# Performance work log

Measured on AMD Instinct MI355X. Metric: run time of the kernel, lower is better.

Reference implementation:

```python
import jax, jax.numpy as jnp
import numpy as np

EPS = 1e-8

@jax.custom_vjp
def spike(x):
    # Heaviside forward, SuperSpike surrogate gradient in backward
    return (x > 0.0).astype(x.dtype)

def _spike_fwd(x):
    return spike(x), x

def _spike_bwd(x, g):
    return (g / (1.0 + 10.0 * jnp.abs(x)) ** 2,)

spike.defvjp(_spike_fwd, _spike_bwd)


def setup_inputs() -> dict:
    key = jax.random.key(0)
    k1, k2, k3, k4 = jax.random.split(key, 4)
    B, T, I, O = 128, 128, 1024, 1024
    x = jax.random.normal(k1, (B, T, I), dtype=jnp.float32)
    # w ~ N(0, 1/sqrt(I)) per reset_parameters
    w = jax.random.normal(k2, (I, O), dtype=jnp.float32) * np.float32(1.0 / np.sqrt(I))
    # beta ~ N(0.7, 0.01), clamped to [0,1]
    beta = jnp.clip(0.7 + 0.01 * jax.random.normal(k3, (1,), dtype=jnp.float32), 0.0, 1.0)
    # b ~ N(1.0, 0.01), clamped to >= 0
    b = jnp.clip(1.0 + 0.01 * jax.random.normal(k4, (1024,), dtype=jnp.float32), 0.0, None)
    return {"x": x, "w": w, "beta": beta, "b": b}


def reference(x, w, beta, b):
    # x: [B, T, I]; w: [I, O]; beta: [1]; b: [O]
    h = jnp.einsum('btc,cd->btd', x, w)                 # [B, T, O]
    d = jnp.einsum('ab,ac->bc', w, w)                    # lateral reset matrix [O, O]
    norm = (w ** 2).sum(0)                               # [O]
    inv_norm = 1.0 / (norm + EPS)
    B, O = x.shape[0], w.shape[1]

    def step(carry, h_t):
        mem, spk = carry
        rst = spk @ d                                    # [B, O]
        mem = (mem - rst) * beta + h_t * (1.0 - beta)
        mthr = mem * inv_norm - b
        spk = spike(mthr)
        return (mem, spk), spk

    init = (jnp.zeros((B, O), x.dtype), jnp.zeros((B, O), x.dtype))
    _, spk_rec = jax.lax.scan(step, init, jnp.swapaxes(h, 0, 1))  # [T, B, O]
    spk_rec = jnp.swapaxes(spk_rec, 0, 1)                # [B, T, O]
    loss = 0.5 * (spk_rec ** 2).mean()
    return spk_rec, loss
```

## Files before the change

kernel.cpp:

```cpp
#include <hip/hip_runtime.h>
#include <hip/hip_fp16.h>

#define B_ 128
#define T_ 128
#define I_ 1024
#define O_ 1024
#define M_ (B_*T_)
#define NOUT (M_*O_)

typedef __attribute__((ext_vector_type(8))) _Float16 half8;
typedef __attribute__((ext_vector_type(4))) float floatx4;

__device__ __forceinline__ void gld_lds16(const void* g, void* l) {
    __builtin_amdgcn_global_load_lds((const __attribute__((address_space(1))) void*)g,
                                     (__attribute__((address_space(3))) void*)l,
                                     16, 0, 0);
}

__device__ __forceinline__ void barrier_lds_only() {
    asm volatile("" ::: "memory");
    __builtin_amdgcn_s_waitcnt(0xC07F);
    __builtin_amdgcn_s_barrier();
    asm volatile("" ::: "memory");
}

__device__ __forceinline__ void split3h(float x, unsigned short& h,
                                        unsigned short& m, unsigned short& l) {
    __half f0 = __float2half(x);
    float r1 = x - __half2float(f0);
    __half f1 = __float2half(r1);
    float r2 = r1 - __half2float(f1);
    __half f2 = __float2half(r2);
    h = __half_as_ushort(f0);
    m = __half_as_ushort(f1);
    l = __half_as_ushort(f2);
}

__global__ __launch_bounds__(256) void split_x(const float* __restrict__ X,
                                               unsigned short* __restrict__ Xh,
                                               unsigned short* __restrict__ Xm,
                                               unsigned short* __restrict__ Xl) {
    size_t base = ((size_t)blockIdx.x * 256 + threadIdx.x) * 4;
    float4 v = *(const float4*)(X + base);
    ushort4 hh, mm, ll;
    split3h(v.x, hh.x, mm.x, ll.x);
    split3h(v.y, hh.y, mm.y, ll.y);
    split3h(v.z, hh.z, mm.z, ll.z);
    split3h(v.w, hh.w, mm.w, ll.w);
    *(ushort4*)(Xh + base) = hh;
    *(ushort4*)(Xm + base) = mm;
    *(ushort4*)(Xl + base) = ll;
}

__global__ __launch_bounds__(256) void split_wt(const float* __restrict__ W,
                                                unsigned short* __restrict__ WTh,
                                                unsigned short* __restrict__ WTm,
                                                unsigned short* __restrict__ WTl) {
    __shared__ float t[64][65];
    const int tid = threadIdx.x;
    const int tx = tid & 63, ty4 = tid >> 6;
    const int r0 = blockIdx.x * 64, c0 = blockIdx.y * 64;
#pragma unroll
    for (int j = 0; j < 16; ++j) {
        int row = j * 4 + ty4;
        t[row][tx] = W[(size_t)(r0 + row) * O_ + c0 + tx];
    }
    __syncthreads();
#pragma unroll
    for (int j = 0; j < 16; ++j) {
        int i = j * 4 + ty4;
        float v = t[tx][i];
        unsigned short h, m, l;
        split3h(v, h, m, l);
        size_t off = (size_t)(c0 + i) * I_ + r0 + tx;
        WTh[off] = h; WTm[off] = m; WTl[off] = l;
    }
}

__global__ __launch_bounds__(512, 2) void gemm_h_mfma(
        const unsigned short* __restrict__ Xh, const unsigned short* __restrict__ Xm,
        const unsigned short* __restrict__ Xl, const unsigned short* __restrict__ WTh,
        const unsigned short* __restrict__ WTm, const unsigned short* __restrict__ WTl,
        float* __restrict__ H) {
    const int K = I_, N = O_;
    __shared__ unsigned short P[2][36864];

    const int tid = threadIdx.x;
    const int lane = tid & 63;
    const int wid = tid >> 6;
    const int wrow = wid >> 2;
    const int wcol = wid & 3;
    const int l15 = lane & 15, quad = lane >> 4;
    const int bm = blockIdx.x * 128, bn = blockIdx.y * 256;

    const int srow = tid >> 2, sch = tid & 3;
    const int schg = sch ^ ((srow >> 1) & 3);
    const unsigned short* gsrcA[3];
    const unsigned short* gsrcB[3];
    gsrcA[0] = Xh  + (size_t)(bm + srow) * K + schg * 8;
    gsrcA[1] = Xm  + (size_t)(bm + srow) * K + schg * 8;
    gsrcA[2] = Xl  + (size_t)(bm + srow) * K + schg * 8;
    gsrcB[0] = WTh + (size_t)(bn + srow) * K + schg * 8;
    gsrcB[1] = WTm + (size_t)(bn + srow) * K + schg * 8;
    gsrcB[2] = WTl + (size_t)(bn + srow) * K + schg * 8;

    auto stage = [&](int kt) {
        unsigned short* wb = &P[0][0] + (size_t)(kt & 1) * 36864;
        const size_t k0 = (size_t)kt * 32;
#pragma unroll
        for (int p = 0; p < 3; ++p)
            gld_lds16(gsrcA[p] + k0, wb + p * 4096 + tid * 8);
#pragma unroll
        for (int p = 0; p < 3; ++p) {
            unsigned short* bb = wb + 12288 + p * 8192 + tid * 8;
            gld_lds16(gsrcB[p] + k0, bb);
            gld_lds16(gsrcB[p] + (size_t)128 * K + k0, bb + 4096);
        }
    };

    floatx4 acc[4][4];
#pragma unroll
    for (int mt = 0; mt < 4; ++mt)
#pragma unroll
        for (int nt = 0; nt < 4; ++nt) acc[mt][nt] = (floatx4)(0.f);

    stage(0);

    for (int kt = 0; kt < 32; ++kt) {
        const unsigned short* rb = &P[0][0] + (size_t)(kt & 1) * 36864;

        asm volatile("" ::: "memory");
        __builtin_amdgcn_s_waitcnt(0x1F70);
        __builtin_amdgcn_s_barrier();
        asm volatile("" ::: "memory");

        half8 Af[3][4];
#pragma unroll
        for (int pa = 0; pa < 3; ++pa)
#pragma unroll
            for (int mt = 0; mt < 4; ++mt) {
                const int row = wrow * 64 + mt * 16 + l15;
                const int chk = quad ^ ((row >> 1) & 3);
                Af[pa][mt] = *(const half8*)(rb + pa * 4096 + row * 32 + chk * 8);
            }

        if (kt < 31) stage(kt + 1);

#pragma unroll
        for (int pb = 0; pb < 3; ++pb) {
            half8 Bf[4];
#pragma unroll
            for (int nt = 0; nt < 4; ++nt) {
                const int col = wcol * 64 + nt * 16 + l15;
                const int chk = quad ^ ((col >> 1) & 3);
                Bf[nt] = *(const half8*)(rb + 12288 + pb * 8192 + col * 32 + chk * 8);
            }
#pragma unroll
            for (int nt = 0; nt < 4; ++nt)
#pragma unroll
                for (int mt = 0; mt < 4; ++mt) {
                    acc[mt][nt] = __builtin_amdgcn_mfma_f32_16x16x32_f16(Af[0][mt], Bf[nt], acc[mt][nt], 0, 0, 0);
                    if (pb < 2)
                        acc[mt][nt] = __builtin_amdgcn_mfma_f32_16x16x32_f16(Af[1][mt], Bf[nt], acc[mt][nt], 0, 0, 0);
                    if (pb == 0)
                        acc[mt][nt] = __builtin_amdgcn_mfma_f32_16x16x32_f16(Af[2][mt], Bf[nt], acc[mt][nt], 0, 0, 0);
                }
        }
    }

#pragma unroll
    for (int mt = 0; mt < 4; ++mt)
#pragma unroll
        for (int nt = 0; nt < 4; ++nt) {
            int grow = bm + wrow * 64 + mt * 16 + quad * 4;
            int gcol = bn + wcol * 64 + nt * 16 + l15;
            float* hp = H + (size_t)grow * N + gcol;
#pragma unroll
            for (int r = 0; r < 4; ++r) hp[(size_t)r * N] = acc[mt][nt][r];
        }
}

__global__ __launch_bounds__(256) void gemm_wtw(const float* __restrict__ W,
                                                float* __restrict__ D) {
    const int K = I_, N = O_;
    __shared__ float As[32][68];
    __shared__ float Bs[32][68];
    const int tid = threadIdx.x;
    const int tx = tid & 15, ty = tid >> 4;
    const int bj = blockIdx.x * 64, bo = blockIdx.y * 64;
    const int lr = tid >> 4;
    const int lc = (tid & 15) << 2;

    float acc[4][4];
#pragma unroll
    for (int m = 0; m < 4; m++)
#pragma unroll
        for (int n = 0; n < 4; n++) acc[m][n] = 0.f;

    for (int k0 = 0; k0 < K; k0 += 32) {
        float4 a0 = *(const float4*)(W + (size_t)(k0 + lr) * N + bj + lc);
        float4 a1 = *(const float4*)(W + (size_t)(k0 + lr + 16) * N + bj + lc);
        float4 b0 = *(const float4*)(W + (size_t)(k0 + lr) * N + bo + lc);
        float4 b1 = *(const float4*)(W + (size_t)(k0 + lr + 16) * N + bo + lc);
        __syncthreads();
        *(float4*)&As[lr][lc] = a0; *(float4*)&As[lr + 16][lc] = a1;
        *(float4*)&Bs[lr][lc] = b0; *(float4*)&Bs[lr + 16][lc] = b1;
        __syncthreads();
#pragma unroll
        for (int k = 0; k < 32; ++k) {
            float4 av = *(const float4*)&As[k][ty * 4];
            float4 bv = *(const float4*)&Bs[k][tx * 4];
            float am[4] = {av.x, av.y, av.z, av.w};
            float bb[4] = {bv.x, bv.y, bv.z, bv.w};
#pragma unroll
            for (int m = 0; m < 4; m++)
#pragma unroll
                for (int n = 0; n < 4; n++) acc[m][n] += am[m] * bb[n];
        }
    }
#pragma unroll
    for (int m = 0; m < 4; m++) {
        float4 v = make_float4(acc[m][0], acc[m][1], acc[m][2], acc[m][3]);
        *(float4*)(D + (size_t)(bj + ty * 4 + m) * N + bo + tx * 4) = v;
    }
}

__global__ void colnorm_diag(const float* __restrict__ D, float* __restrict__ invn,
                             unsigned int* __restrict__ counter,
                             float* __restrict__ zrow) {
    int o = blockIdx.x * 256 + threadIdx.x;
    if (o == 0) *counter = 0u;
    invn[o] = 1.0f / (D[(size_t)o * O_ + o] + 1e-8f);
    zrow[o] = 0.0f;
}

__global__ __launch_bounds__(512) void scan_kernel(const float* __restrict__ h,
                                                   const float* __restrict__ d,
                                                   const float* __restrict__ invn,
                                                   const float* __restrict__ bias,
                                                   const float* __restrict__ beta,
                                                   const float* __restrict__ zrow,
                                                   float* __restrict__ out,
                                                   unsigned int* __restrict__ spike_count) {
    __shared__ int lst[2][O_];
    __shared__ int cnt[T_ + 1];
    __shared__ unsigned int red[512];

    const int tid = threadIdx.x;
    const int lane = tid & 63;
    const int b = blockIdx.x;
    const int o2 = tid * 2;
    const float betav = beta[0];
    const float omb = 1.0f - betav;

    const float2 invn2 = *(const float2*)(invn + o2);
    const float2 b2 = *(const float2*)(bias + o2);
    float2 mem2 = make_float2(0.f, 0.f);

    for (int i = tid; i <= T_; i += 512) cnt[i] = 0;
    unsigned int local_count = 0;
    const float* hb = h + (size_t)b * T_ * O_;
    float* ob = out + (size_t)b * T_ * O_;
    const float* zp = zrow + o2;
    const unsigned long long below = (lane == 63) ? 0xFFFFFFFFFFFFFFFFull >> 1
                                                  : ((1ull << lane) - 1ull);

    float2 hcur = *(const float2*)(hb + o2);
    __syncthreads();

    for (int t = 0; t < T_; ++t) {
        const int p = t & 1, q = p ^ 1;
        const int n = cnt[t];

        float2 hnext = make_float2(0.f, 0.f);
        if (t + 1 < T_) hnext = *(const float2*)(hb + (size_t)(t + 1) * O_ + o2);

        float2 rst = make_float2(0.f, 0.f);
        for (int i = 0; i < n; i += 8) {
            float2 v[8];
#pragma unroll
            for (int u = 0; u < 8; ++u) {
                const int idx = i + u;
                const int j = lst[p][idx & (O_ - 1)];
                const float* src = (idx < n) ? (d + (size_t)j * O_ + o2) : zp;
                v[u] = *(const float2*)src;
            }
#pragma unroll
            for (int u = 0; u < 8; ++u) { rst.x += v[u].x; rst.y += v[u].y; }
        }

        mem2.x = (mem2.x - rst.x) * betav + hcur.x * omb;
        mem2.y = (mem2.y - rst.y) * betav + hcur.y * omb;

        const int s0 = (mem2.x * invn2.x - b2.x) > 0.0f;
        const int s1 = (mem2.y * invn2.y - b2.y) > 0.0f;

        float2 sv = make_float2(s0 ? 1.f : 0.f, s1 ? 1.f : 0.f);
        *(float2*)(ob + (size_t)t * O_ + o2) = sv;
        local_count += (unsigned)(s0 + s1);

        unsigned long long mk0 = __ballot(s0);
        unsigned long long mk1 = __ballot(s1);
        const int c0 = __popcll(mk0);
        const int tot = c0 + __popcll(mk1);
        int base = 0;
        if (lane == 0 && tot) base = atomicAdd(&cnt[t + 1], tot);
        base = __shfl(base, 0, 64);
        if (s0) lst[q][base + __popcll(mk0 & below)] = o2 + 0;
        base += c0;
        if (s1) lst[q][base + __popcll(mk1 & below)] = o2 + 1;

        barrier_lds_only();
        hcur = hnext;
    }

    red[tid] = local_count;
    __syncthreads();
    for (int st = 256; st > 0; st >>= 1) {
        if (tid < st) red[tid] += red[tid + st];
        __syncthreads();
    }
    if (tid == 0) atomicAdd(spike_count, red[0]);
}

__global__ void finalize_loss(const unsigned int* __restrict__ spike_count,
                              float* __restrict__ loss_out) {
    *loss_out = 0.5f * ((float)(*spike_count) / 16777216.0f);
}

extern "C" void kernel_launch(void* const* d_in, const int* in_sizes, int n_in,
                              void* d_out, int out_size, void* d_ws, size_t ws_size,
                              hipStream_t stream) {
    const float* x    = (const float*)d_in[0];
    const float* w    = (const float*)d_in[1];
    const float* beta = (const float*)d_in[2];
    const float* bias = (const float*)d_in[3];
    float* out = (float*)d_out;

    char* ws = (char*)d_ws;
    float* h    = (float*)ws;
    float* dmat = (float*)(ws + (size_t)67108864);
    float* invn = (float*)(ws + (size_t)71303168);
    unsigned int* cntp = (unsigned int*)(ws + (size_t)71307264);
    unsigned short* wt_h = (unsigned short*)(ws + (size_t)71311360);
    unsigned short* wt_m = (unsigned short*)(ws + (size_t)73408512);
    unsigned short* wt_l = (unsigned short*)(ws + (size_t)75505664);
    unsigned short* x_h  = (unsigned short*)(ws + (size_t)77602816);
    unsigned short* x_m  = (unsigned short*)(ws + (size_t)111157248);
    unsigned short* x_l  = (unsigned short*)(ws + (size_t)144711680);
    float* zrow = (float*)x_h;

    split_x<<<M_ * I_ / 1024, 256, 0, stream>>>(x, x_h, x_m, x_l);
    split_wt<<<dim3(I_ / 64, O_ / 64), 256, 0, stream>>>(w, wt_h, wt_m, wt_l);
    gemm_h_mfma<<<dim3(M_ / 128, O_ / 256), 512, 0, stream>>>(x_h, x_m, x_l,
                                                              wt_h, wt_m, wt_l, h);
    gemm_wtw<<<dim3(O_ / 64, O_ / 64), 256, 0, stream>>>(w, dmat);
    colnorm_diag<<<O_ / 256, 256, 0, stream>>>(dmat, invn, cntp, zrow);
    scan_kernel<<<B_, 512, 0, stream>>>(h, dmat, invn, bias, beta, zrow, out, cntp);
    finalize_loss<<<1, 1, 0, stream>>>(cntp, out + (size_t)NOUT);
}
```

Measured before the change: 465.6 us.

## Run scan with one wavefront per batch row using ballot-based spike lists

The scan kernel shrinks from 512 threads per batch row to a single 64-lane wavefront that owns all 1024 outputs (16 per lane). Spike indices are no longer written to an LDS list with atomics and block barriers. Each lane keeps a 16-bit spike mask, and the wave walks the spikes through ballot and readlane. This removes per-timestep block barriers and LDS traffic, but each block now issues far fewer concurrent loads. Only 128 wavefronts cover the whole GPU, so hiding latency on the gathered rows of d gets harder.

```diff
diff --git a/kernel.cpp b/kernel.cpp
--- a/kernel.cpp
+++ b/kernel.cpp
@@ -15,13 +15,6 @@
     __builtin_amdgcn_global_load_lds((const __attribute__((address_space(1))) void*)g,
                                      (__attribute__((address_space(3))) void*)l,
                                      16, 0, 0);
-}
-
-__device__ __forceinline__ void barrier_lds_only() {
-    asm volatile("" ::: "memory");
-    __builtin_amdgcn_s_waitcnt(0xC07F);
-    __builtin_amdgcn_s_barrier();
-    asm volatile("" ::: "memory");
 }
 
 __device__ __forceinline__ void split3h(float x, unsigned short& h,
@@ -234,93 +227,112 @@
     zrow[o] = 0.0f;
 }
 
-__global__ __launch_bounds__(512) void scan_kernel(const float* __restrict__ h,
-                                                   const float* __restrict__ d,
-                                                   const float* __restrict__ invn,
-                                                   const float* __restrict__ bias,
-                                                   const float* __restrict__ beta,
-                                                   const float* __restrict__ zrow,
-                                                   float* __restrict__ out,
-                                                   unsigned int* __restrict__ spike_count) {
-    __shared__ int lst[2][O_];
-    __shared__ int cnt[T_ + 1];
-    __shared__ unsigned int red[512];
-
-    const int tid = threadIdx.x;
-    const int lane = tid & 63;
+__global__ __launch_bounds__(64) void scan_kernel(const float* __restrict__ h,
+                                                  const float* __restrict__ d,
+                                                  const float* __restrict__ invn,
+                                                  const float* __restrict__ bias,
+                                                  const float* __restrict__ beta,
+                                                  const float* __restrict__ zrow,
+                                                  float* __restrict__ out,
+                                                  unsigned int* __restrict__ spike_count) {
+    const int lane = threadIdx.x;
     const int b = blockIdx.x;
-    const int o2 = tid * 2;
     const float betav = beta[0];
     const float omb = 1.0f - betav;
-
-    const float2 invn2 = *(const float2*)(invn + o2);
-    const float2 b2 = *(const float2*)(bias + o2);
-    float2 mem2 = make_float2(0.f, 0.f);
-
-    for (int i = tid; i <= T_; i += 512) cnt[i] = 0;
-    unsigned int local_count = 0;
+    const int base0 = lane * 4;
+
+    float4 mem[4], invn4[4], b4[4], hcur[4], hnext[4];
+#pragma unroll
+    for (int g = 0; g < 4; ++g) {
+        mem[g] = make_float4(0.f, 0.f, 0.f, 0.f);
+        invn4[g] = *(const float4*)(invn + base0 + g * 256);
+        b4[g]   = *(const float4*)(bias + base0 + g * 256);
+    }
     const float* hb = h + (size_t)b * T_ * O_;
     float* ob = out + (size_t)b * T_ * O_;
-    const float* zp = zrow + o2;
-    const unsigned long long below = (lane == 63) ? 0xFFFFFFFFFFFFFFFFull >> 1
-                                                  : ((1ull << lane) - 1ull);
-
-    float2 hcur = *(const float2*)(hb + o2);
-    __syncthreads();
+#pragma unroll
+    for (int g = 0; g < 4; ++g) hcur[g] = *(const float4*)(hb + base0 + g * 256);
+
+    unsigned int lm = 0u;
+    unsigned int local_count = 0u;
 
     for (int t = 0; t < T_; ++t) {
-        const int p = t & 1, q = p ^ 1;
-        const int n = cnt[t];
-
-        float2 hnext = make_float2(0.f, 0.f);
-        if (t + 1 < T_) hnext = *(const float2*)(hb + (size_t)(t + 1) * O_ + o2);
-
-        float2 rst = make_float2(0.f, 0.f);
-        for (int i = 0; i < n; i += 8) {
-            float2 v[8];
-#pragma unroll
-            for (int u = 0; u < 8; ++u) {
-                const int idx = i + u;
-                const int j = lst[p][idx & (O_ - 1)];
-                const float* src = (idx < n) ? (d + (size_t)j * O_ + o2) : zp;
-                v[u] = *(const float2*)src;
+        if (t + 1 < T_) {
+#pragma unroll
+            for (int g = 0; g < 4; ++g)
+                hnext[g] = *(const float4*)(hb + (size_t)(t + 1) * O_ + base0 + g * 256);
+        } else {
+#pragma unroll
+            for (int g = 0; g < 4; ++g) hnext[g] = make_float4(0.f, 0.f, 0.f, 0.f);
+        }
+
+        float4 rst[4];
+#pragma unroll
+        for (int g = 0; g < 4; ++g) rst[g] = make_float4(0.f, 0.f, 0.f, 0.f);
+
+        unsigned long long am = __ballot(lm != 0u);
+        unsigned int cl = 0u;
+        unsigned int clm = 0u;
+        while (am != 0ull || clm != 0u) {
+            const float* srcb[8];
+#pragma unroll
+            for (int k = 0; k < 8; ++k) {
+                while (clm == 0u && am != 0ull) {
+                    cl = (unsigned)__builtin_ctzll(am);
+                    am &= am - 1ull;
+                    clm = (unsigned)__builtin_amdgcn_readlane((int)lm, (int)cl) & 0xFFFFu;
+                }
+                if (clm != 0u) {
+                    const int bbit = __builtin_ctz(clm);
+                    clm &= clm - 1u;
+                    const int j = ((bbit >> 2) << 8) + ((int)cl << 2) + (bbit & 3);
+                    srcb[k] = d + (size_t)j * O_;
+                } else {
+                    srcb[k] = zrow;
+                }
             }
-#pragma unroll
-            for (int u = 0; u < 8; ++u) { rst.x += v[u].x; rst.y += v[u].y; }
-        }
-
-        mem2.x = (mem2.x - rst.x) * betav + hcur.x * omb;
-        mem2.y = (mem2.y - rst.y) * betav + hcur.y * omb;
-
-        const int s0 = (mem2.x * invn2.x - b2.x) > 0.0f;
-        const int s1 = (mem2.y * invn2.y - b2.y) > 0.0f;
-
-        float2 sv = make_float2(s0 ? 1.f : 0.f, s1 ? 1.f : 0.f);
-        *(float2*)(ob + (size_t)t * O_ + o2) = sv;
-        local_count += (unsigned)(s0 + s1);
-
-        unsigned long long mk0 = __ballot(s0);
-        unsigned long long mk1 = __ballot(s1);
-        const int c0 = __popcll(mk0);
-        const int tot = c0 + __popcll(mk1);
-        int base = 0;
-        if (lane == 0 && tot) base = atomicAdd(&cnt[t + 1], tot);
-        base = __shfl(base, 0, 64);
-        if (s0) lst[q][base + __popcll(mk0 & below)] = o2 + 0;
-        base += c0;
-        if (s1) lst[q][base + __popcll(mk1 & below)] = o2 + 1;
-
-        barrier_lds_only();
-        hcur = hnext;
-    }
-
-    red[tid] = local_count;
-    __syncthreads();
-    for (int st = 256; st > 0; st >>= 1) {
-        if (tid < st) red[tid] += red[tid + st];
-        __syncthreads();
-    }
-    if (tid == 0) atomicAdd(spike_count, red[0]);
+            float4 vv[8][4];
+#pragma unroll
+            for (int k = 0; k < 8; ++k)
+#pragma unroll
+                for (int g = 0; g < 4; ++g)
+                    vv[k][g] = *(const float4*)(srcb[k] + base0 + g * 256);
+#pragma unroll
+            for (int k = 0; k < 8; ++k)
+#pragma unroll
+                for (int g = 0; g < 4; ++g) {
+                    rst[g].x += vv[k][g].x; rst[g].y += vv[k][g].y;
+                    rst[g].z += vv[k][g].z; rst[g].w += vv[k][g].w;
+                }
+        }
+
+        unsigned int nlm = 0u;
+#pragma unroll
+        for (int g = 0; g < 4; ++g) {
+            mem[g].x = (mem[g].x - rst[g].x) * betav + hcur[g].x * omb;
+            mem[g].y = (mem[g].y - rst[g].y) * betav + hcur[g].y * omb;
+            mem[g].z = (mem[g].z - rst[g].z) * betav + hcur[g].z * omb;
+            mem[g].w = (mem[g].w - rst[g].w) * betav + hcur[g].w * omb;
+            const int s0 = (mem[g].x * invn4[g].x - b4[g].x) > 0.0f;
+            const int s1 = (mem[g].y * invn4[g].y - b4[g].y) > 0.0f;
+            const int s2 = (mem[g].z * invn4[g].z - b4[g].z) > 0.0f;
+            const int s3 = (mem[g].w * invn4[g].w - b4[g].w) > 0.0f;
+            nlm |= ((unsigned)s0 << (g * 4 + 0)) | ((unsigned)s1 << (g * 4 + 1)) |
+                   ((unsigned)s2 << (g * 4 + 2)) | ((unsigned)s3 << (g * 4 + 3));
+            float4 sv = make_float4(s0 ? 1.f : 0.f, s1 ? 1.f : 0.f,
+                                    s2 ? 1.f : 0.f, s3 ? 1.f : 0.f);
+            *(float4*)(ob + (size_t)t * O_ + base0 + g * 256) = sv;
+            local_count += (unsigned)(s0 + s1 + s2 + s3);
+        }
+        lm = nlm;
+#pragma unroll
+        for (int g = 0; g < 4; ++g) hcur[g] = hnext[g];
+    }
+
+#pragma unroll
+    for (int off = 32; off > 0; off >>= 1)
+        local_count += (unsigned)__shfl_down((int)local_count, off, 64);
+    if (lane == 0) atomicAdd(spike_count, local_count);
 }
 
 __global__ void finalize_loss(const unsigned int* __restrict__ spike_count,
@@ -356,6 +368,6 @@
                                                               wt_h, wt_m, wt_l, h);
     gemm_wtw<<<dim3(O_ / 64, O_ / 64), 256, 0, stream>>>(w, dmat);
     colnorm_diag<<<O_ / 256, 256, 0, stream>>>(dmat, invn, cntp, zrow);
-    scan_kernel<<<B_, 512, 0, stream>>>(h, dmat, invn, bias, beta, zrow, out, cntp);
+    scan_kernel<<<B_, 64, 0, stream>>>(h, dmat, invn, bias, beta, zrow, out, cntp);
     finalize_loss<<<1, 1, 0, stream>>>(cntp, out + (size_t)NOUT);
 }
```

After: 645.7 us. +38.7%, slower.

## Process two batch rows per scan block to share barriers and interleave loads

Applied to the files above, without the earlier changes.

The scan kernel now handles two independent batch rows (b and b+64) in each 512-thread block, launching half as many blocks. The two recurrences are interleaved so the gathered reset-matrix row loads for both can be in flight together, and one barrier per timestep serves both rows. The aim is more memory-level parallelism and fewer barriers across the latency-bound serial scan. The costs are fewer blocks (64 on a many-CU GPU), more registers and LDS per block, and a reset loop whose trip count is the larger of the two spike counts.

```diff
diff --git a/kernel.cpp b/kernel.cpp
--- a/kernel.cpp
+++ b/kernel.cpp
@@ -242,76 +242,109 @@
                                                    const float* __restrict__ zrow,
                                                    float* __restrict__ out,
                                                    unsigned int* __restrict__ spike_count) {
-    __shared__ int lst[2][O_];
-    __shared__ int cnt[T_ + 1];
+    __shared__ int lstA[2][O_], lstB[2][O_];
+    __shared__ int cntA[T_ + 1], cntB[T_ + 1];
     __shared__ unsigned int red[512];
 
     const int tid = threadIdx.x;
     const int lane = tid & 63;
-    const int b = blockIdx.x;
+    const int bA = blockIdx.x;
+    const int bB = blockIdx.x + 64;
     const int o2 = tid * 2;
     const float betav = beta[0];
     const float omb = 1.0f - betav;
 
     const float2 invn2 = *(const float2*)(invn + o2);
     const float2 b2 = *(const float2*)(bias + o2);
-    float2 mem2 = make_float2(0.f, 0.f);
-
-    for (int i = tid; i <= T_; i += 512) cnt[i] = 0;
+    float2 memA = make_float2(0.f, 0.f), memB = make_float2(0.f, 0.f);
+
+    for (int i = tid; i <= T_; i += 512) { cntA[i] = 0; cntB[i] = 0; }
     unsigned int local_count = 0;
-    const float* hb = h + (size_t)b * T_ * O_;
-    float* ob = out + (size_t)b * T_ * O_;
+    const float* hbA = h + (size_t)bA * T_ * O_;
+    const float* hbB = h + (size_t)bB * T_ * O_;
+    float* obA = out + (size_t)bA * T_ * O_;
+    float* obB = out + (size_t)bB * T_ * O_;
     const float* zp = zrow + o2;
     const unsigned long long below = (lane == 63) ? 0xFFFFFFFFFFFFFFFFull >> 1
                                                   : ((1ull << lane) - 1ull);
 
-    float2 hcur = *(const float2*)(hb + o2);
+    float2 hcurA = *(const float2*)(hbA + o2);
+    float2 hcurB = *(const float2*)(hbB + o2);
     __syncthreads();
 
     for (int t = 0; t < T_; ++t) {
         const int p = t & 1, q = p ^ 1;
-        const int n = cnt[t];
-
-        float2 hnext = make_float2(0.f, 0.f);
-        if (t + 1 < T_) hnext = *(const float2*)(hb + (size_t)(t + 1) * O_ + o2);
-
-        float2 rst = make_float2(0.f, 0.f);
-        for (int i = 0; i < n; i += 8) {
-            float2 v[8];
+        const int nA = cntA[t], nB = cntB[t];
+
+        float2 hnextA = make_float2(0.f, 0.f), hnextB = make_float2(0.f, 0.f);
+        if (t + 1 < T_) {
+            hnextA = *(const float2*)(hbA + (size_t)(t + 1) * O_ + o2);
+            hnextB = *(const float2*)(hbB + (size_t)(t + 1) * O_ + o2);
+        }
+
+        float2 rstA = make_float2(0.f, 0.f), rstB = make_float2(0.f, 0.f);
+        const int nmax = (nA > nB) ? nA : nB;
+        for (int i = 0; i < nmax; i += 8) {
+            const float* srcA[8];
+            const float* srcB[8];
 #pragma unroll
             for (int u = 0; u < 8; ++u) {
                 const int idx = i + u;
-                const int j = lst[p][idx & (O_ - 1)];
-                const float* src = (idx < n) ? (d + (size_t)j * O_ + o2) : zp;
-                v[u] = *(const float2*)src;
+                const int jA = lstA[p][idx & (O_ - 1)];
+                const int jB = lstB[p][idx & (O_ - 1)];
+                srcA[u] = (idx < nA) ? (d + (size_t)jA * O_ + o2) : zp;
+                srcB[u] = (idx < nB) ? (d + (size_t)jB * O_ + o2) : zp;
             }
-#pragma unroll
-            for (int u = 0; u < 8; ++u) { rst.x += v[u].x; rst.y += v[u].y; }
-        }
-
-        mem2.x = (mem2.x - rst.x) * betav + hcur.x * omb;
-        mem2.y = (mem2.y - rst.y) * betav + hcur.y * omb;
-
-        const int s0 = (mem2.x * invn2.x - b2.x) > 0.0f;
-        const int s1 = (mem2.y * invn2.y - b2.y) > 0.0f;
-
-        float2 sv = make_float2(s0 ? 1.f : 0.f, s1 ? 1.f : 0.f);
-        *(float2*)(ob + (size_t)t * O_ + o2) = sv;
-        local_count += (unsigned)(s0 + s1);
-
-        unsigned long long mk0 = __ballot(s0);
-        unsigned long long mk1 = __ballot(s1);
-        const int c0 = __popcll(mk0);
-        const int tot = c0 + __popcll(mk1);
-        int base = 0;
-        if (lane == 0 && tot) base = atomicAdd(&cnt[t + 1], tot);
-        base = __shfl(base, 0, 64);
-        if (s0) lst[q][base + __popcll(mk0 & below)] = o2 + 0;
-        base += c0;
-        if (s1) lst[q][base + __popcll(mk1 & below)] = o2 + 1;
+            float2 vA[8], vB[8];
+#pragma unroll
+            for (int u = 0; u < 8; ++u) { vA[u] = *(const float2*)srcA[u];
+                                          vB[u] = *(const float2*)srcB[u]; }
+#pragma unroll
+            for (int u = 0; u < 8; ++u) {
+                rstA.x += vA[u].x; rstA.y += vA[u].y;
+                rstB.x += vB[u].x; rstB.y += vB[u].y;
+            }
+        }
+
+        memA.x = (memA.x - rstA.x) * betav + hcurA.x * omb;
+        memA.y = (memA.y - rstA.y) * betav + hcurA.y * omb;
+        memB.x = (memB.x - rstB.x) * betav + hcurB.x * omb;
+        memB.y = (memB.y - rstB.y) * betav + hcurB.y * omb;
+
+        const int sA0 = (memA.x * invn2.x - b2.x) > 0.0f;
+        const int sA1 = (memA.y * invn2.y - b2.y) > 0.0f;
+        const int sB0 = (memB.x * invn2.x - b2.x) > 0.0f;
+        const int sB1 = (memB.y * invn2.y - b2.y) > 0.0f;
+
+        *(float2*)(obA + (size_t)t * O_ + o2) =
+            make_float2(sA0 ? 1.f : 0.f, sA1 ? 1.f : 0.f);
+        *(float2*)(obB + (size_t)t * O_ + o2) =
+            make_float2(sB0 ? 1.f : 0.f, sB1 ? 1.f : 0.f);
+        local_count += (unsigned)(sA0 + sA1 + sB0 + sB1);
+
+        unsigned long long mA0 = __ballot(sA0);
+        unsigned long long mA1 = __ballot(sA1);
+        unsigned long long mB0 = __ballot(sB0);
+        unsigned long long mB1 = __ballot(sB1);
+        const int cA0 = __popcll(mA0);
+        const int cB0 = __popcll(mB0);
+        const int totA = cA0 + __popcll(mA1);
+        const int totB = cB0 + __popcll(mB1);
+        int baseA = 0, baseB = 0;
+        if (lane == 0) {
+            if (totA) baseA = atomicAdd(&cntA[t + 1], totA);
+            if (totB) baseB = atomicAdd(&cntB[t + 1], totB);
+        }
+        baseA = __shfl(baseA, 0, 64);
+        baseB = __shfl(baseB, 0, 64);
+        if (sA0) lstA[q][baseA + __popcll(mA0 & below)] = o2 + 0;
+        if (sA1) lstA[q][baseA + cA0 + __popcll(mA1 & below)] = o2 + 1;
+        if (sB0) lstB[q][baseB + __popcll(mB0 & below)] = o2 + 0;
+        if (sB1) lstB[q][baseB + cB0 + __popcll(mB1 & below)] = o2 + 1;
 
         barrier_lds_only();
-        hcur = hnext;
+        hcurA = hnextA;
+        hcurB = hnextB;
     }
 
     red[tid] = local_count;
@@ -356,6 +389,6 @@
                                                               wt_h, wt_m, wt_l, h);
     gemm_wtw<<<dim3(O_ / 64, O_ / 64), 256, 0, stream>>>(w, dmat);
     colnorm_diag<<<O_ / 256, 256, 0, stream>>>(dmat, invn, cntp, zrow);
-    scan_kernel<<<B_, 512, 0, stream>>>(h, dmat, invn, bias, beta, zrow, out, cntp);
+    scan_kernel<<<B_ / 2, 512, 0, stream>>>(h, dmat, invn, bias, beta, zrow, out, cntp);
     finalize_loss<<<1, 1, 0, stream>>>(cntp, out + (size_t)NOUT);
 }
```

After: 605.2 us. 1.3x slower.
